# Kernel tuning notes

Measured on AMD Instinct MI355X. Metric: run time of the kernel, lower is better.

## Reference

```python
import jax, jax.numpy as jnp
import numpy as np

D = 384        # model dim
H = 6          # heads
HD = 64        # head dim (inner_dim = H*HD = 384)
DEPTH = 12
P = 16         # patch size
G = 14         # grid side (224/16)
NP = G * G     # 196 patches
NC = 1000
B = 64
DFF = 4 * D
SCALE = HD ** -0.5
EPS = 1e-5


def _ln(x, w, b):
    m = x.mean(-1, keepdims=True)
    v = ((x - m) ** 2).mean(-1, keepdims=True)
    return (x - m) * jax.lax.rsqrt(v + EPS) * w + b


def setup_inputs() -> dict:
    key = jax.random.key(0)
    ks = jax.random.split(key, 16)
    s = 0.02
    inp = {
        "x": jax.random.normal(ks[0], (B, 3, 224, 224), jnp.float32),
        # patch embedding conv as matmul: weight [3*P*P, D]
        "W_patch": jax.random.normal(ks[1], (3 * P * P, D), jnp.float32) * s,
        "b_patch": jnp.zeros((D,), jnp.float32),
        "ln0_w": jnp.ones((D,), jnp.float32),
        "ln0_b": jnp.zeros((D,), jnp.float32),
        "pos_emb": jax.random.normal(ks[2], (1, NP + 1, D), jnp.float32) * s,
        "cls_token": jax.random.normal(ks[3], (1, D), jnp.float32),
        # per-block params stacked over depth
        "ln1_w": jnp.ones((DEPTH, D), jnp.float32),
        "ln1_b": jnp.zeros((DEPTH, D), jnp.float32),
        "Wq": jax.random.normal(ks[4], (DEPTH, D, H * HD), jnp.float32) * s,
        "Wkv": jax.random.normal(ks[5], (DEPTH, D, 2 * H * HD), jnp.float32) * s,
        "Wo": jax.random.normal(ks[6], (DEPTH, H * HD, D), jnp.float32) * s,
        "bo": jnp.zeros((DEPTH, D), jnp.float32),
        "ln2_w": jnp.ones((DEPTH, D), jnp.float32),
        "ln2_b": jnp.zeros((DEPTH, D), jnp.float32),
        "W1": jax.random.normal(ks[7], (DEPTH, D, DFF), jnp.float32) * s,
        "b1": jnp.zeros((DEPTH, DFF), jnp.float32),
        "W2": jax.random.normal(ks[8], (DEPTH, DFF, D), jnp.float32) * s,
        "b2": jnp.zeros((DEPTH, D), jnp.float32),
        "lnf_w": jnp.ones((D,), jnp.float32),
        "lnf_b": jnp.zeros((D,), jnp.float32),
        "Whead": jax.random.normal(ks[9], (D, NC), jnp.float32) * s,
        "bhead": jnp.zeros((NC,), jnp.float32),
    }
    return inp


def reference(x, W_patch, b_patch, ln0_w, ln0_b, pos_emb, cls_token,
              ln1_w, ln1_b, Wq, Wkv, Wo, bo, ln2_w, ln2_b,
              W1, b1, W2, b2, lnf_w, lnf_b, Whead, bhead):
    b = x.shape[0]
    # patch embed: Conv2d(3, D, P, stride=P) == extract patches + matmul
    patches = x.reshape(b, 3, G, P, G, P).transpose(0, 2, 4, 1, 3, 5).reshape(b, NP, 3 * P * P)
    h = patches @ W_patch + b_patch                     # [b, NP, D]
    h = _ln(h, ln0_w, ln0_b)
    cls = jnp.broadcast_to(cls_token[None], (b, 1, D))
    h = jnp.concatenate([cls, h], axis=1) + pos_emb     # [b, NP+1, D]
    n = NP + 1
    for d in range(DEPTH):
        # self-attention with pre-LN, residual
        a = _ln(h, ln1_w[d], ln1_b[d])
        q = (a @ Wq[d]).reshape(b, n, H, HD).transpose(0, 2, 1, 3)
        kv = a @ Wkv[d]
        k = kv[..., : H * HD].reshape(b, n, H, HD).transpose(0, 2, 1, 3)
        v = kv[..., H * HD:].reshape(b, n, H, HD).transpose(0, 2, 1, 3)
        sim = jnp.einsum('bhid,bhjd->bhij', q, k) * SCALE
        attn = jax.nn.softmax(sim, axis=-1)
        o = jnp.einsum('bhij,bhjd->bhid', attn, v)
        o = o.transpose(0, 2, 1, 3).reshape(b, n, H * HD)
        h = h + o @ Wo[d] + bo[d]
        # MLP with pre-LN, residual, exact GELU
        m = _ln(h, ln2_w[d], ln2_b[d])
        m = jax.nn.gelu(m @ W1[d] + b1[d], approximate=False)
        h = h + m @ W2[d] + b2[d]
    cls_out = h[:, 0, :]
    logits = _ln(cls_out, lnf_w, lnf_b) @ Whead + bhead
    return logits
```

## Files before the change

kernel.cpp:

```cpp
#include <hip/hip_runtime.h>


typedef unsigned short u16;
typedef __attribute__((ext_vector_type(8))) short short8;
typedef __attribute__((ext_vector_type(4))) float f32x4;
typedef __attribute__((ext_vector_type(4))) unsigned short u16x4;
typedef __attribute__((ext_vector_type(2))) unsigned short u16x2;

#define D_      384
#define NH      6
#define DEPTH_  12
#define NP_     196
#define NT_     197
#define B_      64
#define DFF_    1536
#define M_REAL  (B_*NT_)
#define M_PAD   12672
#define M_PATCH (B_*NP_)

__device__ __forceinline__ float bf2f(u16 u){
  unsigned int i = ((unsigned int)u) << 16;
  return __builtin_bit_cast(float, i);
}
__device__ __forceinline__ u16 f2bf(float f){
  unsigned int i = __builtin_bit_cast(unsigned int, f);
  i = (i + 0x7FFFu + ((i >> 16) & 1u)) >> 16;
  return (u16)i;
}

#define GLOAD_LDS16(g, l) __builtin_amdgcn_global_load_lds( \
    (const __attribute__((address_space(1))) void*)(g),      \
    (__attribute__((address_space(3))) void*)(l), 16, 0, 0)

#define MFMA_BF16(a, b, c) __builtin_amdgcn_mfma_f32_16x16x32_bf16((a), (b), (c), 0, 0, 0)

__global__ __launch_bounds__(256) void transpose_cvt(const float* __restrict__ src,
                                                     u16* __restrict__ dst, int K, int N,
                                                     int Nsrc,
                                                     size_t sstride, size_t dstride)
{
  __shared__ float tile[32][33];
  src += blockIdx.z * sstride;
  dst += blockIdx.z * dstride;
  int tx = threadIdx.x, ty = threadIdx.y;
  int n0 = blockIdx.x * 32, k0 = blockIdx.y * 32;
#pragma unroll
  for (int i = 0; i < 4; ++i){
    float v = 0.f;
    if (n0 + tx < Nsrc) v = src[(size_t)(k0 + ty + i*8) * Nsrc + n0 + tx];
    tile[ty + i*8][tx] = v;
  }
  __syncthreads();
#pragma unroll
  for (int i = 0; i < 4; ++i)
    dst[(size_t)(n0 + ty + i*8) * K + k0 + tx] = f2bf(tile[tx][ty + i*8]);
}

__global__ __launch_bounds__(256) void patch_extract(const float* __restrict__ x,
                                                     u16* __restrict__ patches)
{
  int r = blockIdx.x;
  int b = r / NP_, p = r % NP_;
  int gy = p / 14, gx = p % 14;
  int t = threadIdx.x;
  int py = t >> 4, px = t & 15;
#pragma unroll
  for (int c = 0; c < 3; ++c){
    float v = x[(((size_t)b*3 + c)*224 + gy*16 + py)*224 + gx*16 + px];
    patches[(size_t)r*768 + c*256 + t] = f2bf(v);
  }
}

template<int MODE, int BM, int BN, int KS>
__global__ __launch_bounds__(256) void gemm_k(const u16* __restrict__ A,
                                              const u16* __restrict__ Bt,
                                              const float* __restrict__ bias,
                                              u16* __restrict__ outb,
                                              float* __restrict__ outf,
                                              int N, int K, int nbx, size_t sstride)
{
  constexpr int MI = BM/32;
  constexpr int NJ = BN/32;
  constexpr int L  = BM/64 + BN/64;
  constexpr int WM = BM/2, WN = BN/2;
  __shared__ u16 lds[3*BM*32 + 3*BN*32];
  u16* As = lds;
  u16* Bs = lds + 3*BM*32;
  int tid = threadIdx.x;
  int w = tid >> 6, lane = tid & 63;

  int nwg = gridDim.x;
  int q = nwg >> 3, r = nwg & 7;
  int xcd = blockIdx.x & 7, slot = blockIdx.x >> 3;
  int wgid = (xcd < r ? xcd*(q+1) : r*(q+1) + (xcd - r)*q) + slot;
  int m0 = (wgid / nbx) * BM;
  int n0 = (wgid % nbx) * BN;
  int kz = (KS > 1) ? blockIdx.y : 0;
  int Kl = K / KS;
  int koff = kz * Kl;
  int wr = w >> 1, wc = w & 1;

  f32x4 acc[MI][NJ];
#pragma unroll
  for (int i = 0; i < MI; ++i)
#pragma unroll
    for (int j = 0; j < NJ; ++j) acc[i][j] = (f32x4){0.f,0.f,0.f,0.f};

  int srow = lane >> 2;
  int skc  = ((lane & 3) ^ (srow & 3)) * 8;
  const u16* Ag = A  + (size_t)(m0 + w*16 + srow) * K + koff + skc;
  const u16* Bg = Bt + (size_t)(n0 + w*16 + srow) * K + koff + skc;

  int fr  = lane & 15;
  int fsw = ((lane >> 4) ^ (lane & 3)) << 3;

  auto stage = [&](int bi, int kt){
    u16* Ad = As + bi*(BM*32) + (w*16)*32;
    u16* Bd = Bs + bi*(BN*32) + (w*16)*32;
#pragma unroll
    for (int c = 0; c < BM/64; ++c)
      GLOAD_LDS16(Ag + (size_t)(c*64)*K + kt, Ad + c*64*32);
#pragma unroll
    for (int c = 0; c < BN/64; ++c)
      GLOAD_LDS16(Bg + (size_t)(c*64)*K + kt, Bd + c*64*32);
  };
  auto compute = [&](int bi){
    const u16* Ab = As + bi*(BM*32);
    const u16* Bb = Bs + bi*(BN*32);
    short8 af[MI], bfr[NJ];
#pragma unroll
    for (int i = 0; i < MI; ++i)
      af[i]  = *(const short8*)&Ab[(wr*WM + i*16 + fr)*32 + fsw];
#pragma unroll
    for (int j = 0; j < NJ; ++j)
      bfr[j] = *(const short8*)&Bb[(wc*WN + j*16 + fr)*32 + fsw];
#pragma unroll
    for (int i = 0; i < MI; ++i)
#pragma unroll
      for (int j = 0; j < NJ; ++j)
        acc[i][j] = MFMA_BF16(af[i], bfr[j], acc[i][j]);
  };

  int nk = Kl >> 5;
  stage(0, 0);
  stage(1, 32);
  int bi = 0;
  for (int t = 0; t < nk - 1; ++t){
    __builtin_amdgcn_sched_barrier(0);
    if constexpr (L == 2)      asm volatile("s_waitcnt vmcnt(2)" ::: "memory");
    else if constexpr (L == 3) asm volatile("s_waitcnt vmcnt(3)" ::: "memory");
    else                       asm volatile("s_waitcnt vmcnt(4)" ::: "memory");
    __builtin_amdgcn_s_barrier();
    asm volatile("" ::: "memory");
    compute(bi);
    if (t + 2 < nk){
      int bs = bi + 2; if (bs >= 3) bs -= 3;
      stage(bs, (t + 2) * 32);
    }
    bi = (bi == 2) ? 0 : bi + 1;
  }
  __builtin_amdgcn_sched_barrier(0);
  asm volatile("s_waitcnt vmcnt(0)" ::: "memory");
  __builtin_amdgcn_s_barrier();
  asm volatile("" ::: "memory");
  compute(bi);

  int cr = (lane >> 4) << 2;
  int cc = lane & 15;

  if constexpr (MODE == 3){
#pragma unroll
    for (int j = 0; j < NJ; ++j){
      int c = n0 + wc*WN + j*16 + cc;
      float bv = bias ? bias[c] : 0.f;
#pragma unroll
      for (int i = 0; i < MI; ++i){
        int rbase = m0 + wr*WM + i*16 + cr;
#pragma unroll
        for (int e = 0; e < 4; ++e){
          float v = acc[i][j][e] + bv;
          if (c < N) outf[(size_t)(rbase + e) * N + c] = v;
        }
      }
    }
  } else {
    __syncthreads();
    constexpr int PITCH = WN + 8;
    u16* Cs = lds + w * (WM * PITCH);
#pragma unroll
    for (int j = 0; j < NJ; ++j){
      int c = n0 + wc*WN + j*16 + cc;
      float bv = (bias && kz == 0) ? bias[c] : 0.f;
#pragma unroll
      for (int i = 0; i < MI; ++i){
#pragma unroll
        for (int e = 0; e < 4; ++e){
          float v = acc[i][j][e] + bv;
          if (MODE == 2) v = 0.5f * v * (1.f + erff(v * 0.70710678118654752f));
          Cs[(i*16 + cr + e) * PITCH + j*16 + cc] = f2bf(v);
        }
      }
    }
    u16* outp = (MODE == 4) ? outb + (size_t)kz * sstride : outb;
    int lr0 = lane >> 3;
    int lc  = lane & 7;
#pragma unroll
    for (int p = 0; p < WM/8; ++p){
      int lr = p*8 + lr0;
      short8 val = *(const short8*)&Cs[lr * PITCH + lc*8];
      size_t gm = (size_t)(m0 + wr*WM + lr);
      *(short8*)&outp[gm * N + n0 + wc*WN + lc*8] = val;
    }
  }
}

__global__ __launch_bounds__(256) void ln_rows(const float* __restrict__ in,
                                               const float* __restrict__ gw,
                                               const float* __restrict__ gb,
                                               u16* __restrict__ out, int rows,
                                               size_t rstride)
{
  int m = blockIdx.x * 4 + (threadIdx.x >> 6);
  int lane = threadIdx.x & 63;
  if (m >= rows) return;
  const float* r = in + (size_t)m * rstride;
  float4 v0 = *(const float4*)(r + lane*4);
  float2 v1 = *(const float2*)(r + 256 + lane*2);
  float sum = v0.x+v0.y+v0.z+v0.w+v1.x+v1.y;
  float sq  = v0.x*v0.x+v0.y*v0.y+v0.z*v0.z+v0.w*v0.w+v1.x*v1.x+v1.y*v1.y;
#pragma unroll
  for (int d = 1; d < 64; d <<= 1){ sum += __shfl_xor(sum, d); sq += __shfl_xor(sq, d); }
  float mean = sum * (1.f/D_);
  float rs = rsqrtf(sq*(1.f/D_) - mean*mean + 1e-5f);
  float4 w0 = *(const float4*)(gw + lane*4);
  float2 w1 = *(const float2*)(gw + 256 + lane*2);
  float4 b0 = *(const float4*)(gb + lane*4);
  float2 b1v= *(const float2*)(gb + 256 + lane*2);
  u16x4 o4 = { f2bf((v0.x-mean)*rs*w0.x + b0.x), f2bf((v0.y-mean)*rs*w0.y + b0.y),
               f2bf((v0.z-mean)*rs*w0.z + b0.z), f2bf((v0.w-mean)*rs*w0.w + b0.w) };
  u16x2 o2 = { f2bf((v1.x-mean)*rs*w1.x + b1v.x), f2bf((v1.y-mean)*rs*w1.y + b1v.y) };
  *(u16x4*)(out + (size_t)m*D_ + lane*4) = o4;
  *(u16x2*)(out + (size_t)m*D_ + 256 + lane*2) = o2;
}

__global__ __launch_bounds__(256) void ln_rows_add(const float* __restrict__ in,
                                                   const u16* __restrict__ s0,
                                                   const u16* __restrict__ s1,
                                                   const float* __restrict__ gw,
                                                   const float* __restrict__ gb,
                                                   u16* __restrict__ out,
                                                   float* __restrict__ hout,
                                                   int rows, size_t rstride)
{
  int m = blockIdx.x * 4 + (threadIdx.x >> 6);
  int lane = threadIdx.x & 63;
  if (m >= rows) return;
  const float* r = in + (size_t)m * rstride;
  const u16* p0 = s0 + (size_t)m * rstride;
  const u16* p1 = s1 + (size_t)m * rstride;
  float4 v0 = *(const float4*)(r + lane*4);
  float2 v1 = *(const float2*)(r + 256 + lane*2);
  u16x4 a0 = *(const u16x4*)(p0 + lane*4);
  u16x2 a1 = *(const u16x2*)(p0 + 256 + lane*2);
  u16x4 c0 = *(const u16x4*)(p1 + lane*4);
  u16x2 c1 = *(const u16x2*)(p1 + 256 + lane*2);
  float x0 = v0.x + bf2f(a0.x) + bf2f(c0.x);
  float x1 = v0.y + bf2f(a0.y) + bf2f(c0.y);
  float x2 = v0.z + bf2f(a0.z) + bf2f(c0.z);
  float x3 = v0.w + bf2f(a0.w) + bf2f(c0.w);
  float x4 = v1.x + bf2f(a1.x) + bf2f(c1.x);
  float x5 = v1.y + bf2f(a1.y) + bf2f(c1.y);
  float sum = x0+x1+x2+x3+x4+x5;
  float sq  = x0*x0+x1*x1+x2*x2+x3*x3+x4*x4+x5*x5;
#pragma unroll
  for (int d = 1; d < 64; d <<= 1){ sum += __shfl_xor(sum, d); sq += __shfl_xor(sq, d); }
  float mean = sum * (1.f/D_);
  float rs = rsqrtf(sq*(1.f/D_) - mean*mean + 1e-5f);
  float4 w0 = *(const float4*)(gw + lane*4);
  float2 w1 = *(const float2*)(gw + 256 + lane*2);
  float4 b0 = *(const float4*)(gb + lane*4);
  float2 b1v= *(const float2*)(gb + 256 + lane*2);
  u16x4 o4 = { f2bf((x0-mean)*rs*w0.x + b0.x), f2bf((x1-mean)*rs*w0.y + b0.y),
               f2bf((x2-mean)*rs*w0.z + b0.z), f2bf((x3-mean)*rs*w0.w + b0.w) };
  u16x2 o2 = { f2bf((x4-mean)*rs*w1.x + b1v.x), f2bf((x5-mean)*rs*w1.y + b1v.y) };
  *(u16x4*)(out + (size_t)m*D_ + lane*4) = o4;
  *(u16x2*)(out + (size_t)m*D_ + 256 + lane*2) = o2;
  if (hout){
    float* ho = hout + (size_t)m * rstride;
    float4 h0 = {x0,x1,x2,x3};
    float2 h1 = {x4,x5};
    *(float4*)(ho + lane*4) = h0;
    *(float2*)(ho + 256 + lane*2) = h1;
  }
}

__global__ __launch_bounds__(256) void assemble_h(const u16* __restrict__ pe,
                                                  const float* __restrict__ gw,
                                                  const float* __restrict__ gb,
                                                  const float* __restrict__ pos,
                                                  const float* __restrict__ cls,
                                                  float* __restrict__ h)
{
  int m = blockIdx.x * 4 + (threadIdx.x >> 6);
  int lane = threadIdx.x & 63;
  if (m >= M_PAD) return;
  float* ho = h + (size_t)m * D_;
  if (m >= M_REAL){
    float4 z = {0.f,0.f,0.f,0.f};
    *(float4*)(ho + lane*4) = z;
    float2 z2 = {0.f,0.f};
    *(float2*)(ho + 256 + lane*2) = z2;
    return;
  }
  int b = m / NT_, t = m % NT_;
  const float* pr = pos + (size_t)t * D_;
  float4 p0 = *(const float4*)(pr + lane*4);
  float2 p1 = *(const float2*)(pr + 256 + lane*2);
  if (t == 0){
    float4 c0 = *(const float4*)(cls + lane*4);
    float2 c1 = *(const float2*)(cls + 256 + lane*2);
    float4 r0 = {c0.x+p0.x, c0.y+p0.y, c0.z+p0.z, c0.w+p0.w};
    float2 r1 = {c1.x+p1.x, c1.y+p1.y};
    *(float4*)(ho + lane*4) = r0;
    *(float2*)(ho + 256 + lane*2) = r1;
  } else {
    const u16* per = pe + (size_t)(b*NP_ + (t-1)) * D_;
    u16x4 a0 = *(const u16x4*)(per + lane*4);
    u16x2 a1 = *(const u16x2*)(per + 256 + lane*2);
    float x0=bf2f(a0.x), x1=bf2f(a0.y), x2=bf2f(a0.z), x3=bf2f(a0.w), x4=bf2f(a1.x), x5=bf2f(a1.y);
    float sum = x0+x1+x2+x3+x4+x5;
    float sq  = x0*x0+x1*x1+x2*x2+x3*x3+x4*x4+x5*x5;
#pragma unroll
    for (int d = 1; d < 64; d <<= 1){ sum += __shfl_xor(sum, d); sq += __shfl_xor(sq, d); }
    float mean = sum * (1.f/D_);
    float rs = rsqrtf(sq*(1.f/D_) - mean*mean + 1e-5f);
    float4 w0 = *(const float4*)(gw + lane*4);
    float2 w1 = *(const float2*)(gw + 256 + lane*2);
    float4 b0 = *(const float4*)(gb + lane*4);
    float2 b1v= *(const float2*)(gb + 256 + lane*2);
    float4 r0 = { (x0-mean)*rs*w0.x + b0.x + p0.x, (x1-mean)*rs*w0.y + b0.y + p0.y,
                  (x2-mean)*rs*w0.z + b0.z + p0.z, (x3-mean)*rs*w0.w + b0.w + p0.w };
    float2 r1 = { (x4-mean)*rs*w1.x + b1v.x + p1.x, (x5-mean)*rs*w1.y + b1v.y + p1.y };
    *(float4*)(ho + lane*4) = r0;
    *(float2*)(ho + 256 + lane*2) = r1;
  }
}

__global__ __launch_bounds__(256) void attn_k(const u16* __restrict__ qkv,
                                              u16* __restrict__ o)
{
  __shared__ u16 Ks[208*72];
  __shared__ u16 Vt[64*232];
  __shared__ u16 Ps[4][16*40];
  int bh = blockIdx.x;
  int b = bh / NH, hh = bh % NH;
  int tid = threadIdx.x, w = tid >> 6, lane = tid & 63;
  const u16* kbase = qkv + (size_t)b*NT_*1152 + 384 + hh*64;
  const u16* vbase = kbase + 384;

  int jr = tid >> 3, col = (tid & 7) * 8;
#pragma unroll
  for (int it = 0; it < 7; ++it){
    int j = it*32 + jr;
    if (j < 208){
      uint4 val = {0u,0u,0u,0u};
      if (j < 197) val = *(const uint4*)(kbase + (size_t)j*1152 + col);
      *(uint4*)&Ks[j*72 + col] = val;
    }
  }
#pragma unroll
  for (int it = 0; it < 7; ++it){
    int j = it*32 + jr;
    union { uint4 v; u16 s[8]; } u;
    u.v.x = 0u; u.v.y = 0u; u.v.z = 0u; u.v.w = 0u;
    if (j < 197) u.v = *(const uint4*)(vbase + (size_t)j*1152 + col);
#pragma unroll
    for (int e = 0; e < 8; ++e) Vt[(size_t)(col+e)*232 + j] = u.s[e];
  }
  __syncthreads();

  u16* myP = Ps[w];
  int fr = lane & 15, fk = lane >> 4;

  for (int qt = w; qt < 13; qt += 4){
    const u16* qrow = qkv + (size_t)(b*NT_ + qt*16 + fr)*1152 + hh*64 + fk*8;
    short8 aq0 = *(const short8*)qrow;
    short8 aq1 = *(const short8*)(qrow + 32);

    f32x4 s[13];
#pragma unroll
    for (int jt = 0; jt < 13; ++jt){
      const u16* kr = &Ks[(jt*16 + fr)*72 + fk*8];
      short8 bk0 = *(const short8*)kr;
      short8 bk1 = *(const short8*)(kr + 32);
      f32x4 z = {0.f,0.f,0.f,0.f};
      z = MFMA_BF16(aq0, bk0, z);
      z = MFMA_BF16(aq1, bk1, z);
      s[jt] = z;
    }

#pragma unroll
    for (int e = 0; e < 4; ++e){
      float mx = -1e30f;
#pragma unroll
      for (int jt = 0; jt < 13; ++jt){
        int cj = jt*16 + fr;
        float v = (cj < NT_) ? s[jt][e]*0.125f : -1e30f;
        s[jt][e] = v;
        mx = fmaxf(mx, v);
      }
#pragma unroll
      for (int d = 1; d < 16; d <<= 1) mx = fmaxf(mx, __shfl_xor(mx, d));
      float su = 0.f;
#pragma unroll
      for (int jt = 0; jt < 13; ++jt){
        float p = __expf(s[jt][e] - mx);
        s[jt][e] = p; su += p;
      }
#pragma unroll
      for (int d = 1; d < 16; d <<= 1) su += __shfl_xor(su, d);
      float ri = 1.f / su;
#pragma unroll
      for (int jt = 0; jt < 13; ++jt) s[jt][e] *= ri;
    }

    f32x4 oacc[4];
#pragma unroll
    for (int dt = 0; dt < 4; ++dt) oacc[dt] = (f32x4){0.f,0.f,0.f,0.f};
#pragma unroll
    for (int jc = 0; jc < 7; ++jc){
#pragma unroll
      for (int jtl = 0; jtl < 2; ++jtl){
        int jt = jc*2 + jtl;
#pragma unroll
        for (int e = 0; e < 4; ++e){
          u16 pv = 0;
          if (jt < 13) pv = f2bf(s[jt][e]);
          myP[(fk*4 + e)*40 + jtl*16 + fr] = pv;
        }
      }
      asm volatile("s_waitcnt lgkmcnt(0)" ::: "memory");
      short8 pa = *(const short8*)&myP[fr*40 + fk*8];
#pragma unroll
      for (int dt = 0; dt < 4; ++dt){
        short8 bv = *(const short8*)&Vt[(size_t)(dt*16 + fr)*232 + jc*32 + fk*8];
        oacc[dt] = MFMA_BF16(pa, bv, oacc[dt]);
      }
    }

#pragma unroll
    for (int dt = 0; dt < 4; ++dt)
#pragma unroll
      for (int e = 0; e < 4; ++e){
        int t = qt*16 + fk*4 + e;
        if (t < NT_)
          o[(size_t)(b*NT_ + t)*384 + hh*64 + dt*16 + fr] = f2bf(oacc[dt][e]);
      }
  }
}

extern "C" void kernel_launch(void* const* d_in, const int* in_sizes, int n_in,
                              void* d_out, int out_size, void* d_ws, size_t ws_size,
                              hipStream_t stream)
{
  (void)in_sizes; (void)n_in; (void)out_size; (void)ws_size;
  const float* x_in    = (const float*)d_in[0];
  const float* W_patch = (const float*)d_in[1];
  const float* b_patch = (const float*)d_in[2];
  const float* ln0_w   = (const float*)d_in[3];
  const float* ln0_b   = (const float*)d_in[4];
  const float* pos_emb = (const float*)d_in[5];
  const float* cls_tok = (const float*)d_in[6];
  const float* ln1_w   = (const float*)d_in[7];
  const float* ln1_b   = (const float*)d_in[8];
  const float* Wq      = (const float*)d_in[9];
  const float* Wkv     = (const float*)d_in[10];
  const float* Wo      = (const float*)d_in[11];
  const float* bo      = (const float*)d_in[12];
  const float* ln2_w   = (const float*)d_in[13];
  const float* ln2_b   = (const float*)d_in[14];
  const float* W1      = (const float*)d_in[15];
  const float* b1      = (const float*)d_in[16];
  const float* W2      = (const float*)d_in[17];
  const float* b2      = (const float*)d_in[18];
  const float* lnf_w   = (const float*)d_in[19];
  const float* lnf_b   = (const float*)d_in[20];
  const float* Whead   = (const float*)d_in[21];
  const float* bhead   = (const float*)d_in[22];

  char* ws = (char*)d_ws;
  size_t off = 0;
  auto nxt = [&](size_t bytes)->char* {
    char* p = ws + off;
    off += (bytes + 255) & ~(size_t)255;
    return p;
  };
  u16*   g_buf   = (u16*)  nxt((size_t)M_PAD * DFF_ * 2);
  float* hbuf    = (float*)nxt((size_t)M_PAD * D_ * 4);
  u16*   abuf    = (u16*)  nxt((size_t)M_PAD * D_ * 2);
  u16*   qkvbuf  = (u16*)  nxt((size_t)M_PAD * 1152 * 2);
  u16*   obuf    = (u16*)  nxt((size_t)M_PAD * D_ * 2);
  u16*   sbuf    = (u16*)  nxt((size_t)2 * M_PAD * D_ * 2);
  u16*   lncls   = (u16*)  nxt((size_t)B_ * D_ * 2);
  u16*   whT     = (u16*)  nxt((size_t)1024 * D_ * 2);
  u16*   wT      = (u16*)  nxt((size_t)21528576 * 2);

  const size_t SS = (size_t)M_PAD * D_;
  u16* patches = g_buf;
  u16* pebuf   = abuf;
  u16* wpT   = wT;
  u16* wqkvT = wpT   + 294912;
  u16* woT   = wqkvT + 12*442368;
  u16* w1T   = woT   + 12*147456;
  u16* w2T   = w1T   + 12*589824;

  dim3 tpb(32, 8);
  transpose_cvt<<<dim3(12, 24, 1),  tpb, 0, stream>>>(W_patch, wpT, 768, 384, 384, 0, 0);
  transpose_cvt<<<dim3(12, 12, 12), tpb, 0, stream>>>(Wq,  wqkvT,            384, 384, 384,
                                                      (size_t)384*384, (size_t)1152*384);
  transpose_cvt<<<dim3(24, 12, 12), tpb, 0, stream>>>(Wkv, wqkvT + 384*384,  384, 768, 768,
                                                      (size_t)384*768, (size_t)1152*384);
  transpose_cvt<<<dim3(12, 12, 12), tpb, 0, stream>>>(Wo,  woT, 384, 384, 384,
                                                      (size_t)384*384, (size_t)384*384);
  transpose_cvt<<<dim3(48, 12, 12), tpb, 0, stream>>>(W1,  w1T, 384, 1536, 1536,
                                                      (size_t)384*1536, (size_t)384*1536);
  transpose_cvt<<<dim3(12, 48, 12), tpb, 0, stream>>>(W2,  w2T, 1536, 384, 384,
                                                      (size_t)1536*384, (size_t)1536*384);
  transpose_cvt<<<dim3(32, 12, 1),  tpb, 0, stream>>>(Whead, whT, 384, 1024, 1000, 0, 0);

  patch_extract<<<M_PATCH, 256, 0, stream>>>(x_in, patches);
  gemm_k<0,64,128,1><<<3*(M_PATCH/64), 256, 0, stream>>>(patches, wpT, b_patch, pebuf, nullptr, 384, 768, 3, 0);
  assemble_h<<<M_PAD/4, 256, 0, stream>>>(pebuf, ln0_w, ln0_b, pos_emb, cls_tok, hbuf);

  for (int d = 0; d < DEPTH_; ++d){
    if (d == 0)
      ln_rows<<<M_PAD/4, 256, 0, stream>>>(hbuf, ln1_w, ln1_b, abuf, M_PAD, D_);
    else
      ln_rows_add<<<M_PAD/4, 256, 0, stream>>>(hbuf, sbuf, sbuf + SS,
                                               ln1_w + d*384, ln1_b + d*384,
                                               abuf, hbuf, M_PAD, D_);
    gemm_k<0,128,128,1><<<9*(M_PAD/128), 256, 0, stream>>>(abuf, wqkvT + (size_t)d*442368, nullptr, qkvbuf, nullptr, 1152, 384, 9, 0);
    attn_k<<<B_*NH, 256, 0, stream>>>(qkvbuf, obuf);
    gemm_k<4,128,128,2><<<dim3(3*(M_PAD/128), 2), 256, 0, stream>>>(obuf, woT + (size_t)d*147456, bo + d*384, sbuf, nullptr, 384, 384, 3, SS);
    ln_rows_add<<<M_PAD/4, 256, 0, stream>>>(hbuf, sbuf, sbuf + SS,
                                             ln2_w + d*384, ln2_b + d*384,
                                             abuf, hbuf, M_PAD, D_);
    gemm_k<2,128,128,1><<<12*(M_PAD/128), 256, 0, stream>>>(abuf, w1T + (size_t)d*589824, b1 + d*1536, g_buf, nullptr, 1536, 384, 12, 0);
    gemm_k<4,128,128,2><<<dim3(3*(M_PAD/128), 2), 256, 0, stream>>>(g_buf, w2T + (size_t)d*589824, b2 + d*384, sbuf, nullptr, 384, 1536, 3, SS);
  }

  ln_rows_add<<<B_/4, 256, 0, stream>>>(hbuf, sbuf, sbuf + SS,
                                        lnf_w, lnf_b, lncls, nullptr,
                                        B_, (size_t)NT_*D_);
  gemm_k<3,64,64,1><<<16, 256, 0, stream>>>(lncls, whT, bhead, nullptr, (float*)d_out, 1000, 384, 16, 0);
}
```

Before: 1.816 ms.

## Switch GEMM to double-buffered LDS, chunked epilogue, and sigmoid-form GELU

```diff
diff --git a/kernel.cpp b/kernel.cpp
--- a/kernel.cpp
+++ b/kernel.cpp
@@ -27,6 +27,10 @@
   i = (i + 0x7FFFu + ((i >> 16) & 1u)) >> 16;
   return (u16)i;
 }
+__device__ __forceinline__ float gelu_f(float x){
+  float t = x * (1.595769122f + 0.0713548162726f * x * x);
+  return x / (1.f + __expf(-t));
+}
 
 #define GLOAD_LDS16(g, l) __builtin_amdgcn_global_load_lds( \
     (const __attribute__((address_space(1))) void*)(g),      \
@@ -83,9 +87,9 @@
   constexpr int NJ = BN/32;
   constexpr int L  = BM/64 + BN/64;
   constexpr int WM = BM/2, WN = BN/2;
-  __shared__ u16 lds[3*BM*32 + 3*BN*32];
+  __shared__ u16 lds[2*(BM+BN)*32];
   u16* As = lds;
-  u16* Bs = lds + 3*BM*32;
+  u16* Bs = lds + 2*BM*32;
   int tid = threadIdx.x;
   int w = tid >> 6, lane = tid & 63;
 
@@ -143,27 +147,23 @@
 
   int nk = Kl >> 5;
   stage(0, 0);
-  stage(1, 32);
-  int bi = 0;
-  for (int t = 0; t < nk - 1; ++t){
+  for (int t = 0; t < nk; ++t){
+    int b = t & 1;
+    if (t + 1 < nk) stage(b ^ 1, (t + 1) * 32);
     __builtin_amdgcn_sched_barrier(0);
-    if constexpr (L == 2)      asm volatile("s_waitcnt vmcnt(2)" ::: "memory");
-    else if constexpr (L == 3) asm volatile("s_waitcnt vmcnt(3)" ::: "memory");
-    else                       asm volatile("s_waitcnt vmcnt(4)" ::: "memory");
+    if (t + 1 < nk){
+      if constexpr (L == 2)      asm volatile("s_waitcnt vmcnt(2)" ::: "memory");
+      else if constexpr (L == 3) asm volatile("s_waitcnt vmcnt(3)" ::: "memory");
+      else                       asm volatile("s_waitcnt vmcnt(4)" ::: "memory");
+    } else {
+      asm volatile("s_waitcnt vmcnt(0)" ::: "memory");
+    }
     __builtin_amdgcn_s_barrier();
     asm volatile("" ::: "memory");
-    compute(bi);
-    if (t + 2 < nk){
-      int bs = bi + 2; if (bs >= 3) bs -= 3;
-      stage(bs, (t + 2) * 32);
-    }
-    bi = (bi == 2) ? 0 : bi + 1;
-  }
-  __builtin_amdgcn_sched_barrier(0);
-  asm volatile("s_waitcnt vmcnt(0)" ::: "memory");
-  __builtin_amdgcn_s_barrier();
-  asm volatile("" ::: "memory");
-  compute(bi);
+    compute(b);
+    __builtin_amdgcn_sched_barrier(0);
+    __builtin_amdgcn_s_barrier();
+  }
 
   int cr = (lane >> 4) << 2;
   int cc = lane & 15;
@@ -184,32 +184,31 @@
       }
     }
   } else {
-    __syncthreads();
     constexpr int PITCH = WN + 8;
-    u16* Cs = lds + w * (WM * PITCH);
-#pragma unroll
-    for (int j = 0; j < NJ; ++j){
-      int c = n0 + wc*WN + j*16 + cc;
-      float bv = (bias && kz == 0) ? bias[c] : 0.f;
-#pragma unroll
-      for (int i = 0; i < MI; ++i){
-#pragma unroll
-        for (int e = 0; e < 4; ++e){
-          float v = acc[i][j][e] + bv;
-          if (MODE == 2) v = 0.5f * v * (1.f + erff(v * 0.70710678118654752f));
-          Cs[(i*16 + cr + e) * PITCH + j*16 + cc] = f2bf(v);
-        }
-      }
-    }
+    u16* Cs = lds + w * (16 * PITCH);
     u16* outp = (MODE == 4) ? outb + (size_t)kz * sstride : outb;
     int lr0 = lane >> 3;
     int lc  = lane & 7;
 #pragma unroll
-    for (int p = 0; p < WM/8; ++p){
-      int lr = p*8 + lr0;
-      short8 val = *(const short8*)&Cs[lr * PITCH + lc*8];
-      size_t gm = (size_t)(m0 + wr*WM + lr);
-      *(short8*)&outp[gm * N + n0 + wc*WN + lc*8] = val;
+    for (int i = 0; i < MI; ++i){
+#pragma unroll
+      for (int j = 0; j < NJ; ++j){
+        int c = n0 + wc*WN + j*16 + cc;
+        float bv = (bias && kz == 0) ? bias[c] : 0.f;
+#pragma unroll
+        for (int e = 0; e < 4; ++e){
+          float v = acc[i][j][e] + bv;
+          if (MODE == 2) v = gelu_f(v);
+          Cs[(cr + e) * PITCH + j*16 + cc] = f2bf(v);
+        }
+      }
+#pragma unroll
+      for (int p = 0; p < 2; ++p){
+        int lr = p*8 + lr0;
+        short8 val = *(const short8*)&Cs[lr * PITCH + lc*8];
+        size_t gm = (size_t)(m0 + wr*WM + i*16 + lr);
+        *(short8*)&outp[gm * N + n0 + wc*WN + lc*8] = val;
+      }
     }
   }
 }
```

Measured after the change: 1.854 ms. 2.1% more time.
